# Performance work log

Measured on AMD Instinct MI355X. Metric: run time of the kernel, lower is better.

Reference implementation:

```python
import jax, jax.numpy as jnp
import numpy as np

S = 8            # n_internal_streams
N = 2**S - 1     # 255 cliques (all non-empty subsets of streams)
D = 32           # half_dim = consciousness_dim // 2
INPUT_DIM = 512
NUM_ITER = 5
B = 1024


def _configs():
    # binary membership of each clique (non-empty subsets), [N, S]
    return ((np.arange(1, 2**S)[:, None] >> np.arange(S)) & 1).astype(np.float32)


def setup_inputs() -> dict:
    key = jax.random.key(0)
    ks = jax.random.split(key, 10)
    cfg = _configs()
    depths = cfg.sum(-1)
    # topological amplitude init: gaussian profile over clique depth
    center, sigma = S / 2.0, S / 3.0
    prof = np.exp(-((depths - center) ** 2) / (2 * sigma ** 2))
    prof = prof / (np.linalg.norm(prof) + 1e-8)
    psi_A0 = jnp.asarray(np.broadcast_to(prof[None, :, None], (1, N, D)).copy(),
                         jnp.float32) + jax.random.normal(ks[0], (1, N, D)) * 0.01
    inp = {
        'network_state': jax.random.normal(ks[1], (B, INPUT_DIM), jnp.float32),
        'W_streams': jax.random.normal(ks[2], (S * D, INPUT_DIM)) / np.sqrt(INPUT_DIM),
        'b_streams': jnp.zeros((S * D,), jnp.float32),
        'W_A': jax.random.normal(ks[3], (D, D)) / np.sqrt(D),
        'b_A': jnp.zeros((D,), jnp.float32),
        'W_phi': jax.random.normal(ks[4], (D, D)) / np.sqrt(D),
        'b_phi': jnp.zeros((D,), jnp.float32),
        'psi_A0': psi_A0,
        'psi_phi0': jax.random.normal(ks[5], (1, N, D)) * 0.3,
        'W_comp': jax.random.normal(ks[6], (32, N)) / np.sqrt(N),
        'b_comp': jnp.zeros((32,), jnp.float32),
        'W_read': jax.random.normal(ks[7], (2 * D, 32 * D)) / np.sqrt(32 * D),
        'b_read': jnp.zeros((2 * D,), jnp.float32),
        'alpha_kin': jnp.asarray(0.5, jnp.float32),
        'mass_sq': jnp.asarray(0.1, jnp.float32),
        'potential_weight': jnp.asarray(0.3, jnp.float32),
        'input_weight': jnp.asarray(0.5, jnp.float32),
        'evolution_rate': jnp.asarray(0.3, jnp.float32),
        'phase_coupling': jnp.asarray(1.0, jnp.float32),
    }
    return inp


def reference(network_state, W_streams, b_streams, W_A, b_A, W_phi, b_phi,
              psi_A0, psi_phi0, W_comp, b_comp, W_read, b_read,
              alpha_kin, mass_sq, potential_weight, input_weight,
              evolution_rate, phase_coupling):
    cfg = jnp.asarray(_configs())                      # [N,S]
    depths = cfg.sum(-1)                               # [N]
    # Hamming-distance kernel between clique configurations
    Ham = cfg @ (1.0 - cfg).T + (1.0 - cfg) @ cfg.T    # [N,N]
    K = jnp.exp(-Ham / S)
    krow = K.sum(1)                                    # [N]

    Bb = network_state.shape[0]
    feats = (network_state @ W_streams.T + b_streams).reshape(Bb, S, D)
    # clique features: mean of member-stream features
    cf = jnp.einsum('ns,bsd->bnd', cfg, feats) / depths[None, :, None]
    A_input = jax.nn.softplus(cf @ W_A.T + b_A)        # [B,N,D]
    phi_input = jnp.pi * jnp.tanh(cf @ W_phi.T + b_phi)

    A = jax.nn.softplus(jnp.broadcast_to(psi_A0, (Bb, N, D)))
    phi = jnp.broadcast_to(psi_phi0, (Bb, N, D))
    dt = jax.nn.sigmoid(evolution_rate)

    for _ in range(NUM_ITER):
        # laplacian: sum_j K_ij (A_j - A_i) / N  (factorized, same math)
        KA = jnp.einsum('ij,bjd->bid', K, A)
        lap = (KA - krow[None, :, None] * A) / N
        sp, cp = jnp.sin(phi), jnp.cos(phi)
        Ks = jnp.einsum('ij,bjd->bid', K, sp)
        Kc = jnp.einsum('ij,bjd->bid', K, cp)
        # sum_j K_ij A_i sin(phi_j - phi_i) / N
        pc = A * (cp * Ks - sp * Kc) / N
        # nonlocal potential: V_i = sum_j K_ij A_j cos(phi_j - phi_i) / N
        KAc = jnp.einsum('ij,bjd->bid', K, A * cp)
        KAs = jnp.einsum('ij,bjd->bid', K, A * sp)
        V = (cp * KAc + sp * KAs) / N
        input_drive = A_input * jnp.sin(phi_input - phi)
        dA = (alpha_kin * lap + potential_weight * V - mass_sq * A
              + input_weight * (A_input - A))
        A = jax.nn.softplus(A + dt * dA)               # updated A used in dphi
        dphi = alpha_kin * pc / (A + 1e-8) + input_weight * input_drive
        phi = phi + dt * dphi
        # per-clique norm clip to 1
        norms = jnp.maximum(jnp.linalg.norm(A, axis=-1, keepdims=True), 1e-8)
        A = A * jnp.where(norms > 1.0, 1.0 / norms, 1.0)

    A_t = jnp.swapaxes(A, 1, 2)                        # [B,D,N]
    Ac = jax.nn.relu(A_t @ W_comp.T + b_comp)          # [B,D,32]
    ro = Ac.reshape(Bb, -1) @ W_read.T + b_read        # [B,2D]
    amplitude = jax.nn.softplus(ro[:, :D])
    phase = jnp.tanh(ro[:, D:] * phase_coupling) * jnp.pi
    psi = (amplitude * jnp.cos(phase)).astype(jnp.complex64) + 1j * (amplitude * jnp.sin(phase)).astype(jnp.complex64)
    return psi, amplitude, phase
```

## Files before the change

kernel.cpp:

```cpp
#include <hip/hip_runtime.h>
#include <math.h>

#define PI_F   3.14159265358979f
#define QF     0.88249690258459546f
#define INV255 (1.0f/255.0f)

__device__ __forceinline__ float softplus_f(float x){
    return fmaxf(x, 0.0f) + __logf(1.0f + __expf(-fabsf(x)));
}
__device__ __forceinline__ float tanh_fast(float x){
    const float e = __expf(2.0f*x);
    return fmaf(-2.0f, __builtin_amdgcn_rcpf(e + 1.0f), 1.0f);
}

template<int CTRL>
__device__ __forceinline__ float dppmov(float x){
    return __int_as_float(__builtin_amdgcn_mov_dpp(__float_as_int(x), CTRL, 0xF, 0xF, false));
}
__device__ __forceinline__ float lxor1 (float x){ return dppmov<0xB1>(x);  }
__device__ __forceinline__ float lxor2 (float x){ return dppmov<0x4E>(x);  }
__device__ __forceinline__ float lxor8 (float x){ return dppmov<0x128>(x); }
__device__ __forceinline__ float lxor4 (float x){ return __int_as_float(__builtin_amdgcn_ds_swizzle(__float_as_int(x), 0x101F)); }
__device__ __forceinline__ float lxor16(float x){ return __int_as_float(__builtin_amdgcn_ds_swizzle(__float_as_int(x), 0x401F)); }
__device__ __forceinline__ float lxor32(float x){ return __shfl_xor(x, 32, 64); }

template<int CTRL>
__device__ __forceinline__ float dppadd(float v){
    return v + __int_as_float(__builtin_amdgcn_update_dpp(0, __float_as_int(v), CTRL, 0xF, 0xF, true));
}
__device__ __forceinline__ float wave_sum63(float v){
    v = dppadd<0x111>(v);
    v = dppadd<0x112>(v);
    v = dppadd<0x114>(v);
    v = dppadd<0x118>(v);
    v = dppadd<0x142>(v);
    v = dppadd<0x143>(v);
    return v;
}

template<int NA>
__device__ __forceinline__ void bflyN(float (&x)[NA][4]){
    const float qv = QF;
    #pragma unroll
    for (int a = 0; a < NA; a++){
        #pragma unroll
        for (int r = 0; r < 4; r++) x[a][r] = fmaf(lxor1 (x[a][r]), qv, x[a][r]);
    }
    #pragma unroll
    for (int a = 0; a < NA; a++){
        #pragma unroll
        for (int r = 0; r < 4; r++) x[a][r] = fmaf(lxor2 (x[a][r]), qv, x[a][r]);
    }
    #pragma unroll
    for (int a = 0; a < NA; a++){
        #pragma unroll
        for (int r = 0; r < 4; r++) x[a][r] = fmaf(lxor8 (x[a][r]), qv, x[a][r]);
    }
    #pragma unroll
    for (int a = 0; a < NA; a++){
        #pragma unroll
        for (int r = 0; r < 4; r++) x[a][r] = fmaf(lxor4 (x[a][r]), qv, x[a][r]);
    }
    #pragma unroll
    for (int a = 0; a < NA; a++){
        #pragma unroll
        for (int r = 0; r < 4; r++) x[a][r] = fmaf(lxor16(x[a][r]), qv, x[a][r]);
    }
    #pragma unroll
    for (int a = 0; a < NA; a++){
        #pragma unroll
        for (int r = 0; r < 4; r++) x[a][r] = fmaf(lxor32(x[a][r]), qv, x[a][r]);
    }
    #pragma unroll
    for (int a = 0; a < NA; a++){
        float t0 = x[a][0], t2 = x[a][2];
        x[a][0] = fmaf(QF, x[a][1], x[a][0]);
        x[a][1] = fmaf(QF, t0,      x[a][1]);
        x[a][2] = fmaf(QF, x[a][3], x[a][2]);
        x[a][3] = fmaf(QF, t2,      x[a][3]);
        t0 = x[a][0]; float t1 = x[a][1];
        x[a][0] = fmaf(QF, x[a][2], x[a][0]);
        x[a][1] = fmaf(QF, x[a][3], x[a][1]);
        x[a][2] = fmaf(QF, t0,      x[a][2]);
        x[a][3] = fmaf(QF, t1,      x[a][3]);
    }
}

__global__ __launch_bounds__(256) void prep_kernel(
        const float* __restrict__ Ws,    const float* __restrict__ psiA0,
        const float* __restrict__ psiP0, const float* __restrict__ p_alpha,
        const float* __restrict__ p_msq, const float* __restrict__ p_pw,
        const float* __restrict__ p_iw,  const float* __restrict__ p_evo,
        float* __restrict__ WsT,  float* __restrict__ Xc,  float* __restrict__ P0c,
        float* __restrict__ F0c)
{
    if (blockIdx.x < 32){
        __shared__ float tile[64][65];
        const int rt = blockIdx.x & 3, ct = blockIdx.x >> 2;
        const int r0 = rt*64, c0t = ct*64;
        const int tx = threadIdx.x & 63, ty = threadIdx.x >> 6;
        #pragma unroll
        for (int k = 0; k < 16; k++){
            const int row = ty*16 + k;
            tile[row][tx] = Ws[(r0+row)*512 + c0t + tx];
        }
        __syncthreads();
        #pragma unroll
        for (int k = 0; k < 16; k++){
            const int row = ty*16 + k;
            WsT[(c0t+row)*256 + r0 + tx] = tile[tx][row];
        }
        return;
    }
    const int tid = threadIdx.x;
    const int w = tid >> 6, l = tid & 63;
    const float alpha = p_alpha[0], msq = p_msq[0], pw = p_pw[0], iw = p_iw[0];
    const float dt   = 1.0f / (1.0f + __expf(-p_evo[0]));
    const float dta  = dt * alpha * INV255;
    const float dtpw = dt * pw * INV255;
    const float c0   = 1.0f - dt * (msq + iw);
    const float m0 = (l == 0) ? 0.0f : 1.0f;
    int nn[4]; float krow[4];
    float c18;
    { const float t1 = 1.0f + QF, t2 = t1*t1, t4 = t2*t2; c18 = t4*t4; }
    #pragma unroll
    for (int r = 0; r < 4; r++){
        nn[r] = l + 64*r;
        krow[r] = c18 - __expf(-0.125f * (float)__popc(nn[r]));
    }
    #pragma unroll
    for (int dd = 0; dd < 8; dd++){
        const int d = w*8 + dd;
        float A0[4], ph0[4], sp[4], cp[4];
        float x[5][4];
        #pragma unroll
        for (int r = 0; r < 4; r++){
            const int n = nn[r];
            A0[r]  = (n > 0) ? softplus_f(psiA0[(n-1)*32 + d]) : 0.0f;
            ph0[r] = (n > 0) ? psiP0[(n-1)*32 + d] : 0.0f;
            sp[r] = __sinf(ph0[r]); cp[r] = __cosf(ph0[r]);
            const float mk = (r == 0) ? m0 : 1.0f;
            const float xa = A0[r] * mk;
            x[0][r] = xa;
            x[1][r] = sp[r] * mk;
            x[2][r] = cp[r] * mk;
            x[3][r] = xa * cp[r];
            x[4][r] = xa * sp[r];
        }
        bflyN<5>(x);
        #pragma unroll
        for (int r = 0; r < 4; r++){
            const float Ao   = A0[r];
            const float lapp = fmaf(-krow[r], Ao, x[0][r]);
            const float Vp   = fmaf(cp[r], x[3][r], sp[r]*x[4][r]);
            const float Pp   = fmaf(-sp[r], x[2][r], cp[r]*x[1][r]);
            float X = c0 * Ao;
            X = fmaf(dta,  lapp, X);
            X = fmaf(dtpw, Vp,   X);
            const int idx = d*256 + nn[r];
            Xc[idx]  = X;
            P0c[idx] = dta * Ao * Pp;
            F0c[idx] = ph0[r];
        }
    }
}

template<bool USET>
__global__ __launch_bounds__(512, 4) void fused_kernel(
        const float* __restrict__ ns,
        const float* __restrict__ Ws,
        const float* __restrict__ WsT,
        const float* __restrict__ bs,
        const float* __restrict__ WA,
        const float* __restrict__ bA,
        const float* __restrict__ WP,
        const float* __restrict__ bP,
        const float* __restrict__ psiA0,
        const float* __restrict__ psiP0,
        const float* __restrict__ Xc,
        const float* __restrict__ P0c,
        const float* __restrict__ F0c,
        const float* __restrict__ Wcomp,
        const float* __restrict__ bcomp,
        const float* __restrict__ Wread,
        const float* __restrict__ bread,
        const float* __restrict__ p_alpha, const float* __restrict__ p_msq,
        const float* __restrict__ p_pw,    const float* __restrict__ p_iw,
        const float* __restrict__ p_evo,   const float* __restrict__ p_pcpl,
        float* __restrict__ out, int Bb)
{
    __shared__ __align__(16) float2 CP[16][512];
    __shared__ __align__(16) float  red[2048];
    __shared__ __align__(16) float  hA[256];
    __shared__ __align__(16) float  hP[256];
    __shared__ __align__(16) float  nsb[512];
    __shared__ __align__(16) float  fe[256];

    float* ac  = red;
    float* rop = red + 1024;

    const int b   = blockIdx.x;
    const int tid = threadIdx.x;
    const int w   = tid >> 6, l = tid & 63;

    const float alpha = p_alpha[0], msq = p_msq[0], pw = p_pw[0], iw = p_iw[0];
    const float pcpl  = p_pcpl[0];
    const float dt    = 1.0f / (1.0f + __expf(-p_evo[0]));
    const float dta  = dt * alpha * INV255;
    const float dtpw = dt * pw * INV255;
    const float c0   = 1.0f - dt * (msq + iw);
    const float dtiw = dt * iw;

    nsb[tid] = ns[b*512 + tid];
    __syncthreads();
    {
        const int k = tid >> 1, part = tid & 1;
        float f = (part == 0) ? bs[k] : 0.0f;
        if (USET){
            const float4* nb4 = (const float4*)nsb + part*64;
            const float*  colb = WsT + (part*64)*1024 + k;
            #pragma unroll 2
            for (int j4 = 0; j4 < 64; j4++){
                const float4 nv = nb4[j4];
                const float* col = colb + j4*1024;
                f = fmaf(col[0],   nv.x, f);
                f = fmaf(col[256], nv.y, f);
                f = fmaf(col[512], nv.z, f);
                f = fmaf(col[768], nv.w, f);
            }
        } else {
            const float4* wr  = (const float4*)(Ws + k*512) + part*64;
            const float4* nb4 = (const float4*)nsb + part*64;
            #pragma unroll 2
            for (int i = 0; i < 64; i++){
                const float4 wv = wr[i], nv = nb4[i];
                f = fmaf(wv.x, nv.x, f); f = fmaf(wv.y, nv.y, f);
                f = fmaf(wv.z, nv.z, f); f = fmaf(wv.w, nv.w, f);
            }
        }
        red[part*256 + k] = f;
    }
    __syncthreads();
    if (tid < 256) fe[tid] = red[tid] + red[256 + tid];
    __syncthreads();
    {
        const int t2 = tid & 255;
        const int s = t2 >> 5, d2 = t2 & 31;
        const float* Wm = (tid < 256) ? WA : WP;
        float acc = 0.0f;
        #pragma unroll 4
        for (int dp = 0; dp < 32; dp++)
            acc = fmaf(Wm[d2*32 + dp], fe[s*32 + dp], acc);
        if (tid < 256) hA[t2] = acc; else hP[t2] = acc;
    }
    __syncthreads();

    int   nn[4];
    float krow[4];
    const float m0 = (l == 0) ? 0.0f : 1.0f;
    float c18;
    { const float t1 = 1.0f + QF, t2 = t1*t1, t4 = t2*t2; c18 = t4*t4; }
    #pragma unroll
    for (int r = 0; r < 4; r++){
        nn[r] = l + 64*r;
        krow[r] = c18 - __expf(-0.125f * (float)__popc(nn[r]));
    }

    float A[4][4], phi[4][4];
    float nrm0[4] = {0.f, 0.f, 0.f, 0.f};

    #pragma unroll
    for (int dd = 0; dd < 4; dd++){
        const int d = w*4 + dd;
        const float bAd = bA[d], bPd = bP[d];
        float gA_[8], gP_[8];
        #pragma unroll
        for (int s = 0; s < 8; s++){ gA_[s] = hA[s*32 + d]; gP_[s] = hP[s*32 + d]; }
        #pragma unroll
        for (int r = 0; r < 4; r++){
            const int pop = __popc(nn[r]);
            const float rdep = 1.0f / (float)(pop ? pop : 1);
            float sA = 0.0f, sP = 0.0f;
            #pragma unroll
            for (int s = 0; s < 8; s++){
                if ((nn[r] >> s) & 1){ sA += gA_[s]; sP += gP_[s]; }
            }
            const float uA  = fmaf(sA, rdep, bAd);
            const float uP  = fmaf(sP, rdep, bPd);
            const float Ain = softplus_f(uA);
            const float pin = PI_F * tanh_fast(uP);
            const float ca = dtiw * Ain;
            CP[dd*4 + r][tid] = make_float2(ca, pin);
            if (USET){
                const int idx = d*256 + nn[r];
                const float An = softplus_f(Xc[idx] + ca);
                const float rr = __builtin_amdgcn_rcpf(An + 1e-8f);
                const float F0 = F0c[idx];
                float pb = fmaf(ca, __sinf(pin - F0), F0);
                phi[dd][r] = fmaf(P0c[idx], rr, pb);
                A[dd][r]   = An;
                nrm0[r]    = fmaf(An, An, nrm0[r]);
            } else {
                const int nm1 = (nn[r] > 0) ? (nn[r] - 1) : 0;
                A[dd][r]   = softplus_f(psiA0[nm1*32 + d]);
                phi[dd][r] = psiP0[nm1*32 + d];
            }
        }
    }

    if (USET){
        #pragma unroll
        for (int r = 0; r < 4; r++) red[w*256 + nn[r]] = nrm0[r];
        __syncthreads();
        float scl[4];
        #pragma unroll
        for (int r = 0; r < 4; r++){
            const int n = nn[r];
            const float t = red[n]        + red[256 + n]  + red[512 + n]  + red[768 + n]
                          + red[1024 + n] + red[1280 + n] + red[1536 + n] + red[1792 + n];
            scl[r] = (t > 1.0f) ? rsqrtf(t) : 1.0f;
        }
        __syncthreads();
        #pragma unroll
        for (int dd = 0; dd < 4; dd++)
            #pragma unroll
            for (int r = 0; r < 4; r++) A[dd][r] *= scl[r];
    }

    const int NFULL = USET ? 3 : 4;
    for (int it = 0; it < NFULL; it++){
        float nrm[4] = {0.f, 0.f, 0.f, 0.f};
        #pragma unroll
        for (int dd = 0; dd < 4; dd++){
            float sp[4], cp[4];
            float x[5][4];
            {
                sp[0] = __sinf(phi[dd][0]); cp[0] = __cosf(phi[dd][0]);
                const float xa = A[dd][0] * m0;
                x[0][0] = xa;
                x[1][0] = sp[0] * m0;
                x[2][0] = cp[0] * m0;
                x[3][0] = xa * cp[0];
                x[4][0] = xa * sp[0];
            }
            #pragma unroll
            for (int r = 1; r < 4; r++){
                sp[r] = __sinf(phi[dd][r]); cp[r] = __cosf(phi[dd][r]);
                const float xa = A[dd][r];
                x[0][r] = xa;
                x[1][r] = sp[r];
                x[2][r] = cp[r];
                x[3][r] = xa * cp[r];
                x[4][r] = xa * sp[r];
            }
            bflyN<5>(x);
            #pragma unroll
            for (int r = 0; r < 4; r++){
                const float2 cpn = CP[dd*4 + r][tid];
                const float Ao   = A[dd][r];
                const float lapp = fmaf(-krow[r], Ao, x[0][r]);
                const float Vp   = fmaf(cp[r], x[3][r], sp[r]*x[4][r]);
                float Aarg = fmaf(c0, Ao, cpn.x);
                Aarg = fmaf(dta,  lapp, Aarg);
                Aarg = fmaf(dtpw, Vp,   Aarg);
                const float An = softplus_f(Aarg);
                const float Pp = fmaf(-sp[r], x[2][r], cp[r]*x[1][r]);
                const float rr = __builtin_amdgcn_rcpf(An + 1e-8f);
                const float sdr = __sinf(cpn.y - phi[dd][r]);
                float pb = fmaf(cpn.x, sdr, phi[dd][r]);
                phi[dd][r] = fmaf(dta*Ao, Pp*rr, pb);
                A[dd][r]   = An;
                nrm[r]     = fmaf(An, An, nrm[r]);
            }
        }
        #pragma unroll
        for (int r = 0; r < 4; r++) red[w*256 + nn[r]] = nrm[r];
        __syncthreads();
        float scl[4];
        #pragma unroll
        for (int r = 0; r < 4; r++){
            const int n = nn[r];
            const float t = red[n]        + red[256 + n]  + red[512 + n]  + red[768 + n]
                          + red[1024 + n] + red[1280 + n] + red[1536 + n] + red[1792 + n];
            scl[r] = (t > 1.0f) ? rsqrtf(t) : 1.0f;
        }
        __syncthreads();
        #pragma unroll
        for (int dd = 0; dd < 4; dd++)
            #pragma unroll
            for (int r = 0; r < 4; r++) A[dd][r] *= scl[r];
    }

    {
        float nrm[4] = {0.f, 0.f, 0.f, 0.f};
        #pragma unroll
        for (int dd = 0; dd < 4; dd++){
            float sp[4], cp[4];
            float y[3][4];
            {
                sp[0] = __sinf(phi[dd][0]); cp[0] = __cosf(phi[dd][0]);
                const float xa = A[dd][0] * m0;
                y[0][0] = xa;
                y[1][0] = xa * cp[0];
                y[2][0] = xa * sp[0];
            }
            #pragma unroll
            for (int r = 1; r < 4; r++){
                sp[r] = __sinf(phi[dd][r]); cp[r] = __cosf(phi[dd][r]);
                const float xa = A[dd][r];
                y[0][r] = xa;
                y[1][r] = xa * cp[r];
                y[2][r] = xa * sp[r];
            }
            bflyN<3>(y);
            #pragma unroll
            for (int r = 0; r < 4; r++){
                const float Ao   = A[dd][r];
                const float lapp = fmaf(-krow[r], Ao, y[0][r]);
                const float Vp   = fmaf(cp[r], y[1][r], sp[r]*y[2][r]);
                float Aarg = fmaf(c0, Ao, CP[dd*4 + r][tid].x);
                Aarg = fmaf(dta,  lapp, Aarg);
                Aarg = fmaf(dtpw, Vp,   Aarg);
                const float An = softplus_f(Aarg);
                A[dd][r]   = An;
                nrm[r]     = fmaf(An, An, nrm[r]);
            }
        }
        #pragma unroll
        for (int r = 0; r < 4; r++) red[w*256 + nn[r]] = nrm[r];
        __syncthreads();
        float scl[4];
        #pragma unroll
        for (int r = 0; r < 4; r++){
            const int n = nn[r];
            const float t = red[n]        + red[256 + n]  + red[512 + n]  + red[768 + n]
                          + red[1024 + n] + red[1280 + n] + red[1536 + n] + red[1792 + n];
            scl[r] = (t > 1.0f) ? rsqrtf(t) : 1.0f;
        }
        __syncthreads();
        #pragma unroll
        for (int dd = 0; dd < 4; dd++)
            #pragma unroll
            for (int r = 0; r < 4; r++) A[dd][r] *= scl[r];
    }

    #pragma unroll
    for (int dd = 0; dd < 4; dd++) A[dd][0] *= m0;

    for (int c = 0; c < 32; c++){
        float wv[4];
        #pragma unroll
        for (int r = 0; r < 4; r++){
            const int idx = c*255 + nn[r] - 1;
            wv[r] = Wcomp[idx < 0 ? 0 : idx];
        }
        const float bc = bcomp[c];
        #pragma unroll
        for (int dd = 0; dd < 4; dd++){
            float v = wv[0] * A[dd][0];
            v = fmaf(wv[1], A[dd][1], v);
            v = fmaf(wv[2], A[dd][2], v);
            v = fmaf(wv[3], A[dd][3], v);
            v = wave_sum63(v);
            if (l == 63)
                ac[(w*4 + dd)*32 + c] = fmaxf(v + bc, 0.0f);
        }
    }
    __syncthreads();

    {
        const int k = tid >> 2, part = tid & 3;
        const float4* Wr4 = (const float4*)Wread + k*256;
        const float4* ac4 = (const float4*)ac;
        float s = 0.0f;
        #pragma unroll 2
        for (int jj = 0; jj < 64; jj++){
            const int j4 = part + 4*jj;
            const float4 wv = Wr4[j4];
            const float4 av = ac4[j4];
            s = fmaf(wv.x, av.x, s); s = fmaf(wv.y, av.y, s);
            s = fmaf(wv.z, av.z, s); s = fmaf(wv.w, av.w, s);
        }
        rop[tid] = s;
    }
    __syncthreads();
    if (tid < 32){
        const float ra = rop[tid*4] + rop[tid*4+1] + rop[tid*4+2] + rop[tid*4+3] + bread[tid];
        const int   t2 = tid + 32;
        const float rp = rop[t2*4] + rop[t2*4+1] + rop[t2*4+2] + rop[t2*4+3] + bread[t2];
        const float amp = softplus_f(ra);
        const float ph  = PI_F * tanhf(rp * pcpl);
        const float cph = __cosf(ph);
        const int o = b*32 + tid;
        out[o]         = amp * cph;
        out[Bb*32 + o] = amp;
        out[Bb*64 + o] = ph;
    }
}

extern "C" void kernel_launch(void* const* d_in, const int* in_sizes, int n_in,
                              void* d_out, int out_size, void* d_ws, size_t ws_size,
                              hipStream_t stream) {
    const float* ns      = (const float*)d_in[0];
    const float* Ws      = (const float*)d_in[1];
    const float* bs      = (const float*)d_in[2];
    const float* WA      = (const float*)d_in[3];
    const float* bA      = (const float*)d_in[4];
    const float* WP      = (const float*)d_in[5];
    const float* bP      = (const float*)d_in[6];
    const float* psiA0   = (const float*)d_in[7];
    const float* psiP0   = (const float*)d_in[8];
    const float* Wcomp   = (const float*)d_in[9];
    const float* bcomp   = (const float*)d_in[10];
    const float* Wread   = (const float*)d_in[11];
    const float* bread   = (const float*)d_in[12];
    const float* p_alpha = (const float*)d_in[13];
    const float* p_msq   = (const float*)d_in[14];
    const float* p_pw    = (const float*)d_in[15];
    const float* p_iw    = (const float*)d_in[16];
    const float* p_evo   = (const float*)d_in[17];
    const float* p_pcpl  = (const float*)d_in[18];

    const int Bb = in_sizes[0] / 512;

    const size_t need = (size_t)(512*256 + 3*32*256) * sizeof(float);
    if (ws_size >= need){
        float* WsT = (float*)d_ws;
        float* Xc  = WsT + 512*256;
        float* P0c = Xc  + 32*256;
        float* F0c = P0c + 32*256;
        prep_kernel<<<33, 256, 0, stream>>>(Ws, psiA0, psiP0,
                                            p_alpha, p_msq, p_pw, p_iw, p_evo,
                                            WsT, Xc, P0c, F0c);
        fused_kernel<true><<<Bb, 512, 0, stream>>>(ns, Ws, WsT, bs, WA, bA, WP, bP,
                                                   psiA0, psiP0, Xc, P0c, F0c,
                                                   Wcomp, bcomp, Wread, bread,
                                                   p_alpha, p_msq, p_pw, p_iw,
                                                   p_evo, p_pcpl, (float*)d_out, Bb);
    } else {
        fused_kernel<false><<<Bb, 512, 0, stream>>>(ns, Ws, nullptr, bs, WA, bA, WP, bP,
                                                    psiA0, psiP0,
                                                    nullptr, nullptr, nullptr,
                                                    Wcomp, bcomp, Wread, bread,
                                                    p_alpha, p_msq, p_pw, p_iw,
                                                    p_evo, p_pcpl, (float*)d_out, Bb);
    }
}
```

Baseline: 303.0 us.

## Keep evolving A/phi state in LDS, drive-term constants in registers, defer norm scaling

The per-thread A and phi state arrays (16+16 floats) move into shared memory, and the input-drive constants (ca, pin) move from shared memory into registers. The norm-clip scale is applied lazily when state is reloaded instead of rescaling every element after each iteration. sched_barriers limit cross-dd scheduling, and several loop unroll factors are raised. The intent appears to be lower register pressure and possibly better occupancy, at the cost of extra LDS traffic every iteration.

Result: faster. 286.1 us (-5.6%).

```diff
diff --git a/kernel.cpp b/kernel.cpp
--- a/kernel.cpp
+++ b/kernel.cpp
@@ -189,7 +189,7 @@
         const float* __restrict__ p_evo,   const float* __restrict__ p_pcpl,
         float* __restrict__ out, int Bb)
 {
-    __shared__ __align__(16) float2 CP[16][512];
+    __shared__ __align__(16) float2 ST[16][512];
     __shared__ __align__(16) float  red[2048];
     __shared__ __align__(16) float  hA[256];
     __shared__ __align__(16) float  hP[256];
@@ -219,7 +219,7 @@
         if (USET){
             const float4* nb4 = (const float4*)nsb + part*64;
             const float*  colb = WsT + (part*64)*1024 + k;
-            #pragma unroll 2
+            #pragma unroll 8
             for (int j4 = 0; j4 < 64; j4++){
                 const float4 nv = nb4[j4];
                 const float* col = colb + j4*1024;
@@ -231,7 +231,7 @@
         } else {
             const float4* wr  = (const float4*)(Ws + k*512) + part*64;
             const float4* nb4 = (const float4*)nsb + part*64;
-            #pragma unroll 2
+            #pragma unroll 8
             for (int i = 0; i < 64; i++){
                 const float4 wv = wr[i], nv = nb4[i];
                 f = fmaf(wv.x, nv.x, f); f = fmaf(wv.y, nv.y, f);
@@ -248,7 +248,7 @@
         const int s = t2 >> 5, d2 = t2 & 31;
         const float* Wm = (tid < 256) ? WA : WP;
         float acc = 0.0f;
-        #pragma unroll 4
+        #pragma unroll 8
         for (int dp = 0; dp < 32; dp++)
             acc = fmaf(Wm[d2*32 + dp], fe[s*32 + dp], acc);
         if (tid < 256) hA[t2] = acc; else hP[t2] = acc;
@@ -266,7 +266,8 @@
         krow[r] = c18 - __expf(-0.125f * (float)__popc(nn[r]));
     }
 
-    float A[4][4], phi[4][4];
+    float CAp[4][4], Pin[4][4];
+    float scl_c[4] = {1.0f, 1.0f, 1.0f, 1.0f};
     float nrm0[4] = {0.f, 0.f, 0.f, 0.f};
 
     #pragma unroll
@@ -290,41 +291,36 @@
             const float Ain = softplus_f(uA);
             const float pin = PI_F * tanh_fast(uP);
             const float ca = dtiw * Ain;
-            CP[dd*4 + r][tid] = make_float2(ca, pin);
+            CAp[dd][r] = ca; Pin[dd][r] = pin;
             if (USET){
                 const int idx = d*256 + nn[r];
                 const float An = softplus_f(Xc[idx] + ca);
                 const float rr = __builtin_amdgcn_rcpf(An + 1e-8f);
                 const float F0 = F0c[idx];
                 float pb = fmaf(ca, __sinf(pin - F0), F0);
-                phi[dd][r] = fmaf(P0c[idx], rr, pb);
-                A[dd][r]   = An;
-                nrm0[r]    = fmaf(An, An, nrm0[r]);
+                ST[dd*4 + r][tid] = make_float2(An, fmaf(P0c[idx], rr, pb));
+                nrm0[r] = fmaf(An, An, nrm0[r]);
             } else {
                 const int nm1 = (nn[r] > 0) ? (nn[r] - 1) : 0;
-                A[dd][r]   = softplus_f(psiA0[nm1*32 + d]);
-                phi[dd][r] = psiP0[nm1*32 + d];
-            }
-        }
+                ST[dd*4 + r][tid] = make_float2(softplus_f(psiA0[nm1*32 + d]),
+                                                psiP0[nm1*32 + d]);
+            }
+        }
+        __builtin_amdgcn_sched_barrier(0);
     }
 
     if (USET){
         #pragma unroll
         for (int r = 0; r < 4; r++) red[w*256 + nn[r]] = nrm0[r];
         __syncthreads();
-        float scl[4];
         #pragma unroll
         for (int r = 0; r < 4; r++){
             const int n = nn[r];
             const float t = red[n]        + red[256 + n]  + red[512 + n]  + red[768 + n]
                           + red[1024 + n] + red[1280 + n] + red[1536 + n] + red[1792 + n];
-            scl[r] = (t > 1.0f) ? rsqrtf(t) : 1.0f;
-        }
-        __syncthreads();
-        #pragma unroll
-        for (int dd = 0; dd < 4; dd++)
-            #pragma unroll
-            for (int r = 0; r < 4; r++) A[dd][r] *= scl[r];
+            scl_c[r] = (t > 1.0f) ? rsqrtf(t) : 1.0f;
+        }
+        __syncthreads();
     }
 
     const int NFULL = USET ? 3 : 4;
@@ -332,11 +328,17 @@
         float nrm[4] = {0.f, 0.f, 0.f, 0.f};
         #pragma unroll
         for (int dd = 0; dd < 4; dd++){
-            float sp[4], cp[4];
+            float Al[4], ph[4], sp[4], cp[4];
+            #pragma unroll
+            for (int r = 0; r < 4; r++){
+                const float2 st = ST[dd*4 + r][tid];
+                Al[r] = st.x * scl_c[r];
+                ph[r] = st.y;
+            }
             float x[5][4];
             {
-                sp[0] = __sinf(phi[dd][0]); cp[0] = __cosf(phi[dd][0]);
-                const float xa = A[dd][0] * m0;
+                sp[0] = __sinf(ph[0]); cp[0] = __cosf(ph[0]);
+                const float xa = Al[0] * m0;
                 x[0][0] = xa;
                 x[1][0] = sp[0] * m0;
                 x[2][0] = cp[0] * m0;
@@ -345,8 +347,8 @@
             }
             #pragma unroll
             for (int r = 1; r < 4; r++){
-                sp[r] = __sinf(phi[dd][r]); cp[r] = __cosf(phi[dd][r]);
-                const float xa = A[dd][r];
+                sp[r] = __sinf(ph[r]); cp[r] = __cosf(ph[r]);
+                const float xa = Al[r];
                 x[0][r] = xa;
                 x[1][r] = sp[r];
                 x[2][r] = cp[r];
@@ -356,58 +358,58 @@
             bflyN<5>(x);
             #pragma unroll
             for (int r = 0; r < 4; r++){
-                const float2 cpn = CP[dd*4 + r][tid];
-                const float Ao   = A[dd][r];
+                const float Ao   = Al[r];
                 const float lapp = fmaf(-krow[r], Ao, x[0][r]);
                 const float Vp   = fmaf(cp[r], x[3][r], sp[r]*x[4][r]);
-                float Aarg = fmaf(c0, Ao, cpn.x);
+                float Aarg = fmaf(c0, Ao, CAp[dd][r]);
                 Aarg = fmaf(dta,  lapp, Aarg);
                 Aarg = fmaf(dtpw, Vp,   Aarg);
                 const float An = softplus_f(Aarg);
                 const float Pp = fmaf(-sp[r], x[2][r], cp[r]*x[1][r]);
                 const float rr = __builtin_amdgcn_rcpf(An + 1e-8f);
-                const float sdr = __sinf(cpn.y - phi[dd][r]);
-                float pb = fmaf(cpn.x, sdr, phi[dd][r]);
-                phi[dd][r] = fmaf(dta*Ao, Pp*rr, pb);
-                A[dd][r]   = An;
-                nrm[r]     = fmaf(An, An, nrm[r]);
-            }
+                const float sdr = __sinf(Pin[dd][r] - ph[r]);
+                float pb = fmaf(CAp[dd][r], sdr, ph[r]);
+                ST[dd*4 + r][tid] = make_float2(An, fmaf(dta*Ao, Pp*rr, pb));
+                nrm[r] = fmaf(An, An, nrm[r]);
+            }
+            __builtin_amdgcn_sched_barrier(0);
         }
         #pragma unroll
         for (int r = 0; r < 4; r++) red[w*256 + nn[r]] = nrm[r];
         __syncthreads();
-        float scl[4];
         #pragma unroll
         for (int r = 0; r < 4; r++){
             const int n = nn[r];
             const float t = red[n]        + red[256 + n]  + red[512 + n]  + red[768 + n]
                           + red[1024 + n] + red[1280 + n] + red[1536 + n] + red[1792 + n];
-            scl[r] = (t > 1.0f) ? rsqrtf(t) : 1.0f;
-        }
-        __syncthreads();
-        #pragma unroll
-        for (int dd = 0; dd < 4; dd++)
-            #pragma unroll
-            for (int r = 0; r < 4; r++) A[dd][r] *= scl[r];
+            scl_c[r] = (t > 1.0f) ? rsqrtf(t) : 1.0f;
+        }
+        __syncthreads();
     }
 
     {
         float nrm[4] = {0.f, 0.f, 0.f, 0.f};
         #pragma unroll
         for (int dd = 0; dd < 4; dd++){
-            float sp[4], cp[4];
+            float Al[4], ph[4], sp[4], cp[4];
+            #pragma unroll
+            for (int r = 0; r < 4; r++){
+                const float2 st = ST[dd*4 + r][tid];
+                Al[r] = st.x * scl_c[r];
+                ph[r] = st.y;
+            }
             float y[3][4];
             {
-                sp[0] = __sinf(phi[dd][0]); cp[0] = __cosf(phi[dd][0]);
-                const float xa = A[dd][0] * m0;
+                sp[0] = __sinf(ph[0]); cp[0] = __cosf(ph[0]);
+                const float xa = Al[0] * m0;
                 y[0][0] = xa;
                 y[1][0] = xa * cp[0];
                 y[2][0] = xa * sp[0];
             }
             #pragma unroll
             for (int r = 1; r < 4; r++){
-                sp[r] = __sinf(phi[dd][r]); cp[r] = __cosf(phi[dd][r]);
-                const float xa = A[dd][r];
+                sp[r] = __sinf(ph[r]); cp[r] = __cosf(ph[r]);
+                const float xa = Al[r];
                 y[0][r] = xa;
                 y[1][r] = xa * cp[r];
                 y[2][r] = xa * sp[r];
@@ -415,37 +417,39 @@
             bflyN<3>(y);
             #pragma unroll
             for (int r = 0; r < 4; r++){
-                const float Ao   = A[dd][r];
+                const float Ao   = Al[r];
                 const float lapp = fmaf(-krow[r], Ao, y[0][r]);
                 const float Vp   = fmaf(cp[r], y[1][r], sp[r]*y[2][r]);
-                float Aarg = fmaf(c0, Ao, CP[dd*4 + r][tid].x);
+                float Aarg = fmaf(c0, Ao, CAp[dd][r]);
                 Aarg = fmaf(dta,  lapp, Aarg);
                 Aarg = fmaf(dtpw, Vp,   Aarg);
                 const float An = softplus_f(Aarg);
-                A[dd][r]   = An;
-                nrm[r]     = fmaf(An, An, nrm[r]);
-            }
+                ST[dd*4 + r][tid] = make_float2(An, 0.0f);
+                nrm[r] = fmaf(An, An, nrm[r]);
+            }
+            __builtin_amdgcn_sched_barrier(0);
         }
         #pragma unroll
         for (int r = 0; r < 4; r++) red[w*256 + nn[r]] = nrm[r];
         __syncthreads();
-        float scl[4];
         #pragma unroll
         for (int r = 0; r < 4; r++){
             const int n = nn[r];
             const float t = red[n]        + red[256 + n]  + red[512 + n]  + red[768 + n]
                           + red[1024 + n] + red[1280 + n] + red[1536 + n] + red[1792 + n];
-            scl[r] = (t > 1.0f) ? rsqrtf(t) : 1.0f;
-        }
-        __syncthreads();
-        #pragma unroll
-        for (int dd = 0; dd < 4; dd++)
-            #pragma unroll
-            for (int r = 0; r < 4; r++) A[dd][r] *= scl[r];
-    }
-
-    #pragma unroll
-    for (int dd = 0; dd < 4; dd++) A[dd][0] *= m0;
+            scl_c[r] = (t > 1.0f) ? rsqrtf(t) : 1.0f;
+        }
+        __syncthreads();
+    }
+
+    float Ar[4][4];
+    #pragma unroll
+    for (int dd = 0; dd < 4; dd++){
+        #pragma unroll
+        for (int r = 0; r < 4; r++)
+            Ar[dd][r] = ST[dd*4 + r][tid].x * scl_c[r];
+        Ar[dd][0] *= m0;
+    }
 
     for (int c = 0; c < 32; c++){
         float wv[4];
@@ -457,10 +461,10 @@
         const float bc = bcomp[c];
         #pragma unroll
         for (int dd = 0; dd < 4; dd++){
-            float v = wv[0] * A[dd][0];
-            v = fmaf(wv[1], A[dd][1], v);
-            v = fmaf(wv[2], A[dd][2], v);
-            v = fmaf(wv[3], A[dd][3], v);
+            float v = wv[0] * Ar[dd][0];
+            v = fmaf(wv[1], Ar[dd][1], v);
+            v = fmaf(wv[2], Ar[dd][2], v);
+            v = fmaf(wv[3], Ar[dd][3], v);
             v = wave_sum63(v);
             if (l == 63)
                 ac[(w*4 + dd)*32 + c] = fmaxf(v + bc, 0.0f);
@@ -473,7 +477,7 @@
         const float4* Wr4 = (const float4*)Wread + k*256;
         const float4* ac4 = (const float4*)ac;
         float s = 0.0f;
-        #pragma unroll 2
+        #pragma unroll 4
         for (int jj = 0; jj < 64; jj++){
             const int j4 = part + 4*jj;
             const float4 wv = Wr4[j4];
```
